# Optimization experiments

Hardware: AMD Instinct MI355X
Metric: run time of the kernel (lower is better)

Reference implementation:

```python
import jax, jax.numpy as jnp
import numpy as np

N = 50000      # nodes
E = 800000     # edges (before self loops)
F_IN = 256     # input features
C = 64         # out_channels per head
H = 4          # heads
NC = 3         # num_class


def setup_inputs() -> dict:
    key = jax.random.key(0)
    ks = jax.random.split(key, 11)
    s = 0.1
    return {
        "x": jax.random.normal(ks[0], (N, F_IN), jnp.float32),
        "edge_index": jax.random.randint(ks[1], (2, E), 0, N, dtype=jnp.int64),
        # conv1: in=F_IN -> H*C, concat
        "W1": jax.random.normal(ks[2], (H * C, F_IN), jnp.float32) * s,
        "as1": jax.random.normal(ks[3], (H, C), jnp.float32) * s,
        "ad1": jax.random.normal(ks[4], (H, C), jnp.float32) * s,
        "b1": jnp.zeros((H * C,), jnp.float32),
        # conv2: in=H*C -> H*C, concat
        "W2": jax.random.normal(ks[5], (H * C, H * C), jnp.float32) * s,
        "as2": jax.random.normal(ks[6], (H, C), jnp.float32) * s,
        "ad2": jax.random.normal(ks[7], (H, C), jnp.float32) * s,
        "b2": jnp.zeros((H * C,), jnp.float32),
        # conv3: in=H*C -> NC, heads averaged (concat=False)
        "W3": jax.random.normal(ks[8], (H * NC, H * C), jnp.float32) * s,
        "as3": jax.random.normal(ks[9], (H, NC), jnp.float32) * s,
        "ad3": jax.random.normal(ks[10], (H, NC), jnp.float32) * s,
        "b3": jnp.zeros((NC,), jnp.float32),
    }


def _gat_conv(x, src, dst, W, a_src, a_dst, b, concat):
    # x: [N,F]; src/dst: [E'] (self loops included); W: [H*C, F]; a_*: [H,C]
    n = x.shape[0]
    h_, c_ = a_src.shape
    h = (x @ W.T).reshape(n, h_, c_)                       # [N,H,C]
    alpha_src = (h * a_src[None]).sum(-1)                  # [N,H]
    alpha_dst = (h * a_dst[None]).sum(-1)                  # [N,H]
    e = jax.nn.leaky_relu(alpha_src[src] + alpha_dst[dst], 0.2)  # [E',H]
    # segment softmax over destination-node neighborhoods
    m = jax.ops.segment_max(e, dst, num_segments=n)        # [N,H]
    ex = jnp.exp(e - m[dst])
    den = jax.ops.segment_sum(ex, dst, num_segments=n)     # [N,H]
    alpha = ex / den[dst]                                  # [E',H]
    out = jax.ops.segment_sum(h[src] * alpha[:, :, None], dst, num_segments=n)  # [N,H,C]
    if concat:
        return out.reshape(n, h_ * c_) + b
    return out.mean(axis=1) + b


def reference(x, edge_index, W1, as1, ad1, b1, W2, as2, ad2, b2, W3, as3, ad3, b3):
    n = x.shape[0]
    loop = jnp.arange(n, dtype=edge_index.dtype)
    src = jnp.concatenate([edge_index[0], loop])  # add_self_loops=True
    dst = jnp.concatenate([edge_index[1], loop])
    x = jax.nn.elu(_gat_conv(x, src, dst, W1, as1, ad1, b1, True))
    x = jax.nn.elu(_gat_conv(x, src, dst, W2, as2, ad2, b2, True))
    x = jax.nn.elu(_gat_conv(x, src, dst, W3, as3, ad3, b3, False))
    return x
```

## Files before the change

kernel.cpp:

```cpp
#include <hip/hip_runtime.h>
#include <hip/hip_fp16.h>
#include <cstdint>
#include <cstddef>

#define NNODES 50000
#define NEDGES 800000
#define E2 (NEDGES + NNODES)
#define HC 256

typedef __attribute__((ext_vector_type(8))) short short8v;
typedef __attribute__((ext_vector_type(4))) float f32x4;


__global__ void zero_int(int* __restrict__ p, int n) {
    int i = blockIdx.x * 256 + threadIdx.x;
    if (i < n) p[i] = 0;
}

__global__ void count_deg(const int* __restrict__ ei, int* __restrict__ deg) {
    int i = blockIdx.x * 256 + threadIdx.x;
    if (i >= E2) return;
    int d = (i < NEDGES) ? ei[NEDGES + i] : (i - NEDGES);
    atomicAdd(&deg[d], 1);
}

__global__ void scan1(const int* __restrict__ deg, int* __restrict__ rp, int* __restrict__ bs) {
    __shared__ int s[256];
    int t = threadIdx.x, i = blockIdx.x * 256 + t;
    int v = (i < NNODES) ? deg[i] : 0;
    s[t] = v;
    __syncthreads();
    for (int o = 1; o < 256; o <<= 1) {
        int add = (t >= o) ? s[t - o] : 0;
        __syncthreads();
        s[t] += add;
        __syncthreads();
    }
    if (i < NNODES) rp[i] = s[t] - v;
    if (t == 255) bs[blockIdx.x] = s[255];
}

__global__ void scan2(int* __restrict__ bs, int nb) {
    __shared__ int s[256];
    int t = threadIdx.x;
    int v = (t < nb) ? bs[t] : 0;
    s[t] = v;
    __syncthreads();
    for (int o = 1; o < 256; o <<= 1) {
        int add = (t >= o) ? s[t - o] : 0;
        __syncthreads();
        s[t] += add;
        __syncthreads();
    }
    bs[t] = s[t] - v;
}

__global__ void scan3(int* __restrict__ rp, const int* __restrict__ bs, int* __restrict__ cnt) {
    int i = blockIdx.x * 256 + threadIdx.x;
    if (i < NNODES) {
        int v = rp[i] + bs[blockIdx.x];
        rp[i] = v;
        cnt[i] = v;
    }
    if (i == 0) rp[NNODES] = E2;
}

__global__ void fill_csr(const int* __restrict__ ei, int* __restrict__ cnt, int* __restrict__ csr) {
    int i = blockIdx.x * 256 + threadIdx.x;
    if (i >= E2) return;
    int s, d;
    if (i < NEDGES) { s = ei[i]; d = ei[NEDGES + i]; }
    else            { s = d = i - NEDGES; }
    int pos = atomicAdd(&cnt[d], 1);
    csr[pos] = s;
}


__device__ __forceinline__ unsigned short f2bf(float f) {
    uint32_t u = __float_as_uint(f);
    uint32_t r = (u + 0x7FFFu + ((u >> 16) & 1u)) >> 16;
    return (unsigned short)r;
}
__device__ __forceinline__ float bf2f(unsigned short h) {
    return __uint_as_float(((uint32_t)h) << 16);
}

__global__ void split_bf16(const float* __restrict__ in, unsigned short* __restrict__ hi,
                           unsigned short* __restrict__ lo, int n4) {
    int i = blockIdx.x * 256 + threadIdx.x;
    if (i >= n4) return;
    float4 v = ((const float4*)in)[i];
    unsigned short h0 = f2bf(v.x), h1 = f2bf(v.y), h2 = f2bf(v.z), h3 = f2bf(v.w);
    unsigned short l0 = f2bf(v.x - bf2f(h0));
    unsigned short l1 = f2bf(v.y - bf2f(h1));
    unsigned short l2 = f2bf(v.z - bf2f(h2));
    unsigned short l3 = f2bf(v.w - bf2f(h3));
    uint2 hp, lp;
    hp.x = (uint32_t)h0 | ((uint32_t)h1 << 16);
    hp.y = (uint32_t)h2 | ((uint32_t)h3 << 16);
    lp.x = (uint32_t)l0 | ((uint32_t)l1 << 16);
    lp.y = (uint32_t)l2 | ((uint32_t)l3 << 16);
    *(uint2*)(hi + 4 * (size_t)i) = hp;
    *(uint2*)(lo + 4 * (size_t)i) = lp;
}


__global__ __launch_bounds__(256, 2) void gemm_mfma(
    const unsigned short* __restrict__ Ah, const unsigned short* __restrict__ Al,
    const unsigned short* __restrict__ Wh, const unsigned short* __restrict__ Wl,
    float* __restrict__ out, _Float16* __restrict__ out16, int M) {
    __shared__ unsigned short sAh[128][32], sAl[128][32], sWh[128][32], sWl[128][32];
    const int t = threadIdx.x;
    const int m0 = blockIdx.x * 128, n0 = blockIdx.y * 128;
    const int lane = t & 63, w = t >> 6;
    const int wr = w >> 1, wc = w & 1;
    const int fr = lane & 15, fg = lane >> 4;

    f32x4 acc[4][4];
#pragma unroll
    for (int mi = 0; mi < 4; mi++)
#pragma unroll
        for (int ni = 0; ni < 4; ni++) acc[mi][ni] = (f32x4){0.f, 0.f, 0.f, 0.f};

    for (int kc = 0; kc < 256; kc += 32) {
#pragma unroll
        for (int i = 0; i < 2; i++) {
            int u = t + 256 * i;
            int row = u >> 2;
            int cb = (u & 3) * 8;
            int gra = m0 + row; gra = gra < M ? gra : M - 1;
            int grw = n0 + row;
            *(short8v*)&sAh[row][cb] = *(const short8v*)(Ah + (size_t)gra * HC + kc + cb);
            *(short8v*)&sAl[row][cb] = *(const short8v*)(Al + (size_t)gra * HC + kc + cb);
            *(short8v*)&sWh[row][cb] = *(const short8v*)(Wh + (size_t)grw * HC + kc + cb);
            *(short8v*)&sWl[row][cb] = *(const short8v*)(Wl + (size_t)grw * HC + kc + cb);
        }
        __syncthreads();

        short8v ah[4], al[4], bh[4], bl[4];
#pragma unroll
        for (int i = 0; i < 4; i++) {
            ah[i] = *(const short8v*)&sAh[wr * 64 + i * 16 + fr][fg * 8];
            al[i] = *(const short8v*)&sAl[wr * 64 + i * 16 + fr][fg * 8];
            bh[i] = *(const short8v*)&sWh[wc * 64 + i * 16 + fr][fg * 8];
            bl[i] = *(const short8v*)&sWl[wc * 64 + i * 16 + fr][fg * 8];
        }
#pragma unroll
        for (int mi = 0; mi < 4; mi++)
#pragma unroll
            for (int ni = 0; ni < 4; ni++) {
                acc[mi][ni] = __builtin_amdgcn_mfma_f32_16x16x32_bf16(ah[mi], bh[ni], acc[mi][ni], 0, 0, 0);
                acc[mi][ni] = __builtin_amdgcn_mfma_f32_16x16x32_bf16(ah[mi], bl[ni], acc[mi][ni], 0, 0, 0);
                acc[mi][ni] = __builtin_amdgcn_mfma_f32_16x16x32_bf16(al[mi], bh[ni], acc[mi][ni], 0, 0, 0);
            }
        __syncthreads();
    }

#pragma unroll
    for (int mi = 0; mi < 4; mi++) {
#pragma unroll
        for (int r = 0; r < 4; r++) {
            int gr = m0 + wr * 64 + mi * 16 + fg * 4 + r;
            if (gr < M) {
#pragma unroll
                for (int ni = 0; ni < 4; ni++) {
                    float v = acc[mi][ni][r];
                    size_t off = (size_t)gr * HC + n0 + wc * 64 + ni * 16 + fr;
                    out[off] = v;
                    out16[off] = (_Float16)v;
                }
            }
        }
    }
}


__global__ void alpha_hc(const float* __restrict__ h, const float* __restrict__ a_s,
                         const float* __restrict__ a_d, float* __restrict__ asrc,
                         float* __restrict__ adst) {
    int n = blockIdx.x;
    int t = threadIdx.x;
    float v = h[(size_t)n * HC + t];
    float ps = v * a_s[t];
    float pd = v * a_d[t];
    for (int o = 32; o > 0; o >>= 1) {
        ps += __shfl_xor(ps, o);
        pd += __shfl_xor(pd, o);
    }
    if ((t & 63) == 0) {
        int w = t >> 6;
        asrc[n * 4 + w] = ps;
        adst[n * 4 + w] = pd;
    }
}


#define CHUNK 512

__global__ void aggregate_hc(const _Float16* __restrict__ h16, const float* __restrict__ asrc,
                             const float* __restrict__ adst, const int* __restrict__ rp,
                             const int* __restrict__ csr, const float* __restrict__ bias,
                             float* __restrict__ y) {
    __shared__ int   sIdx[CHUNK];
    __shared__ float sE[4][CHUNK];
    int n = blockIdx.x;
    int t = threadIdx.x;
    int w = t >> 6, l = t & 63;
    int r0 = rp[n], deg = rp[n + 1] - r0;
    float ad = adst[n * 4 + w];
    int hoff = (w << 6) + l;
    const _Float16* hp = h16 + hoff;

    if (deg <= CHUNK) {
        for (int j = t; j < deg; j += 256) sIdx[j] = csr[r0 + j];
        __syncthreads();

        float m = -1e30f;
        for (int j = l; j < deg; j += 64) {
            int s = sIdx[j];
            float e = asrc[s * 4 + w] + ad;
            e = e > 0.f ? e : 0.2f * e;
            sE[w][j] = e;
            m = fmaxf(m, e);
        }
#pragma unroll
        for (int o = 32; o > 0; o >>= 1) m = fmaxf(m, __shfl_xor(m, o));

        float ssum = 0.f;
        for (int j = l; j < deg; j += 64) {
            float ex = __expf(sE[w][j] - m);
            sE[w][j] = ex;
            ssum += ex;
        }
#pragma unroll
        for (int o = 32; o > 0; o >>= 1) ssum += __shfl_xor(ssum, o);

        float acc = 0.f;
        int j = 0;
        for (; j + 4 <= deg; j += 4) {
            int s0 = sIdx[j], s1 = sIdx[j + 1], s2 = sIdx[j + 2], s3 = sIdx[j + 3];
            float a0 = sE[w][j], a1 = sE[w][j + 1], a2 = sE[w][j + 2], a3 = sE[w][j + 3];
            float h0 = (float)hp[(size_t)s0 * HC];
            float h1 = (float)hp[(size_t)s1 * HC];
            float h2 = (float)hp[(size_t)s2 * HC];
            float h3v = (float)hp[(size_t)s3 * HC];
            acc = fmaf(a0, h0, acc);
            acc = fmaf(a1, h1, acc);
            acc = fmaf(a2, h2, acc);
            acc = fmaf(a3, h3v, acc);
        }
        for (; j < deg; j++) {
            acc = fmaf(sE[w][j], (float)hp[(size_t)sIdx[j] * HC], acc);
        }

        float outv = acc / ssum + bias[hoff];
        outv = outv > 0.f ? outv : expm1f(outv);
        y[(size_t)n * HC + hoff] = outv;
    } else {
        float m = -1e30f;
        for (int j = l; j < deg; j += 64) {
            int s = csr[r0 + j];
            float e = asrc[s * 4 + w] + ad;
            e = e > 0.f ? e : 0.2f * e;
            m = fmaxf(m, e);
        }
#pragma unroll
        for (int o = 32; o > 0; o >>= 1) m = fmaxf(m, __shfl_xor(m, o));

        float acc = 0.f, ssum = 0.f;
        for (int j = 0; j < deg; j++) {
            int s = csr[r0 + j];
            float e = asrc[s * 4 + w] + ad;
            e = e > 0.f ? e : 0.2f * e;
            float a = __expf(e - m);
            ssum += a;
            acc = fmaf(a, (float)hp[(size_t)s * HC], acc);
        }
        float outv = acc / ssum + bias[hoff];
        outv = outv > 0.f ? outv : expm1f(outv);
        y[(size_t)n * HC + hoff] = outv;
    }
}


__global__ void gemm_small(const float* __restrict__ Y, const float* __restrict__ W3,
                           float* __restrict__ h3) {
    int idx = blockIdx.x * 256 + threadIdx.x;
    if (idx >= NNODES * 12) return;
    int n = idx / 12, o = idx - n * 12;
    const float4* xr = (const float4*)(Y + (size_t)n * HC);
    const float4* wr = (const float4*)(W3 + o * HC);
    float acc = 0.f;
#pragma unroll 8
    for (int k = 0; k < 64; k++) {
        float4 a = xr[k], b = wr[k];
        acc += a.x * b.x + a.y * b.y + a.z * b.z + a.w * b.w;
    }
    h3[idx] = acc;
}

__global__ void alpha3(const float* __restrict__ h3, const float* __restrict__ a_s,
                       const float* __restrict__ a_d, float* __restrict__ asrc,
                       float* __restrict__ adst) {
    int n = blockIdx.x * 256 + threadIdx.x;
    if (n >= NNODES) return;
    const float* hr = h3 + (size_t)n * 12;
    float s[4], d[4];
#pragma unroll
    for (int hh = 0; hh < 4; hh++) {
        s[hh] = hr[hh * 3] * a_s[hh * 3] + hr[hh * 3 + 1] * a_s[hh * 3 + 1] + hr[hh * 3 + 2] * a_s[hh * 3 + 2];
        d[hh] = hr[hh * 3] * a_d[hh * 3] + hr[hh * 3 + 1] * a_d[hh * 3 + 1] + hr[hh * 3 + 2] * a_d[hh * 3 + 2];
    }
    *(float4*)(asrc + n * 4) = make_float4(s[0], s[1], s[2], s[3]);
    *(float4*)(adst + n * 4) = make_float4(d[0], d[1], d[2], d[3]);
}

__global__ void aggregate3(const float* __restrict__ h3, const float* __restrict__ asrc,
                           const float* __restrict__ adst, const int* __restrict__ rp,
                           const int* __restrict__ csr, const float* __restrict__ b3,
                           float* __restrict__ out) {
    int n = blockIdx.x * 4 + (threadIdx.x >> 6);
    int l = threadIdx.x & 63;
    if (n >= NNODES) return;
    int r0 = rp[n], deg = rp[n + 1] - r0;
    float4 ad = *(const float4*)(adst + n * 4);

    float m0 = -1e30f, m1 = -1e30f, m2 = -1e30f, m3 = -1e30f;
    for (int j = l; j < deg; j += 64) {
        int s = csr[r0 + j];
        float4 a4 = *(const float4*)(asrc + s * 4);
        float e0 = a4.x + ad.x, e1 = a4.y + ad.y, e2 = a4.z + ad.z, e3 = a4.w + ad.w;
        e0 = e0 > 0.f ? e0 : 0.2f * e0;
        e1 = e1 > 0.f ? e1 : 0.2f * e1;
        e2 = e2 > 0.f ? e2 : 0.2f * e2;
        e3 = e3 > 0.f ? e3 : 0.2f * e3;
        m0 = fmaxf(m0, e0); m1 = fmaxf(m1, e1); m2 = fmaxf(m2, e2); m3 = fmaxf(m3, e3);
    }
    for (int o = 32; o > 0; o >>= 1) {
        m0 = fmaxf(m0, __shfl_xor(m0, o));
        m1 = fmaxf(m1, __shfl_xor(m1, o));
        m2 = fmaxf(m2, __shfl_xor(m2, o));
        m3 = fmaxf(m3, __shfl_xor(m3, o));
    }

    float acc[12];
#pragma unroll
    for (int k = 0; k < 12; k++) acc[k] = 0.f;
    float s0 = 0.f, s1 = 0.f, s2 = 0.f, s3 = 0.f;
    for (int j = l; j < deg; j += 64) {
        int s = csr[r0 + j];
        float4 a4 = *(const float4*)(asrc + s * 4);
        float e0 = a4.x + ad.x, e1 = a4.y + ad.y, e2 = a4.z + ad.z, e3 = a4.w + ad.w;
        e0 = e0 > 0.f ? e0 : 0.2f * e0;
        e1 = e1 > 0.f ? e1 : 0.2f * e1;
        e2 = e2 > 0.f ? e2 : 0.2f * e2;
        e3 = e3 > 0.f ? e3 : 0.2f * e3;
        float w0 = __expf(e0 - m0), w1 = __expf(e1 - m1), w2 = __expf(e2 - m2), w3 = __expf(e3 - m3);
        s0 += w0; s1 += w1; s2 += w2; s3 += w3;
        const float* hr = h3 + (size_t)s * 12;
#pragma unroll
        for (int c = 0; c < 3; c++) {
            acc[c]     += w0 * hr[c];
            acc[3 + c] += w1 * hr[3 + c];
            acc[6 + c] += w2 * hr[6 + c];
            acc[9 + c] += w3 * hr[9 + c];
        }
    }
    for (int o = 32; o > 0; o >>= 1) {
#pragma unroll
        for (int k = 0; k < 12; k++) acc[k] += __shfl_xor(acc[k], o);
        s0 += __shfl_xor(s0, o);
        s1 += __shfl_xor(s1, o);
        s2 += __shfl_xor(s2, o);
        s3 += __shfl_xor(s3, o);
    }
    if (l < 3) {
        float v = 0.25f * (acc[l] / s0 + acc[3 + l] / s1 + acc[6 + l] / s2 + acc[9 + l] / s3) + b3[l];
        v = v > 0.f ? v : expm1f(v);
        out[(size_t)n * 3 + l] = v;
    }
}


extern "C" void kernel_launch(void* const* d_in, const int* in_sizes, int n_in,
                              void* d_out, int out_size, void* d_ws, size_t ws_size,
                              hipStream_t stream) {
    (void)in_sizes; (void)n_in; (void)out_size; (void)ws_size;
    const float* x   = (const float*)d_in[0];
    const int*   ei  = (const int*)d_in[1];
    const float* W1  = (const float*)d_in[2];
    const float* as1 = (const float*)d_in[3];
    const float* ad1 = (const float*)d_in[4];
    const float* b1  = (const float*)d_in[5];
    const float* W2  = (const float*)d_in[6];
    const float* as2 = (const float*)d_in[7];
    const float* ad2 = (const float*)d_in[8];
    const float* b2  = (const float*)d_in[9];
    const float* W3  = (const float*)d_in[10];
    const float* as3 = (const float*)d_in[11];
    const float* ad3 = (const float*)d_in[12];
    const float* b3  = (const float*)d_in[13];
    float* out = (float*)d_out;

    uint8_t* p = (uint8_t*)d_ws;
    auto alloc = [&](size_t bytes) -> void* {
        void* r = (void*)p;
        p += (bytes + 255) & ~(size_t)255;
        return r;
    };
    float* bufH = (float*)alloc((size_t)NNODES * HC * 4);
    float* bufY = (float*)alloc((size_t)NNODES * HC * 4);
    float* h3   = (float*)alloc((size_t)NNODES * 12 * 4);
    float* asrc = (float*)alloc((size_t)NNODES * 4 * 4);
    float* adst = (float*)alloc((size_t)NNODES * 4 * 4);
    int* deg    = (int*)alloc((size_t)NNODES * 4);
    int* rp     = (int*)alloc((size_t)(NNODES + 1) * 4);
    int* cnt    = (int*)alloc((size_t)NNODES * 4);
    int* csr    = (int*)alloc((size_t)E2 * 4);
    int* bsums  = (int*)alloc(256 * 4);
    unsigned short* xh  = (unsigned short*)alloc((size_t)NNODES * HC * 2);
    unsigned short* xl  = (unsigned short*)alloc((size_t)NNODES * HC * 2);
    unsigned short* w1h = (unsigned short*)alloc((size_t)HC * HC * 2);
    unsigned short* w1l = (unsigned short*)alloc((size_t)HC * HC * 2);
    unsigned short* w2h = (unsigned short*)alloc((size_t)HC * HC * 2);
    unsigned short* w2l = (unsigned short*)alloc((size_t)HC * HC * 2);
    _Float16* h16 = (_Float16*)alloc((size_t)NNODES * HC * 2);

    const int NB_N = (NNODES + 255) / 256;
    const int NB_E = (E2 + 255) / 256;
    const int N4_A = NNODES * HC / 4;
    const int N4_W = HC * HC / 4;

    zero_int<<<NB_N, 256, 0, stream>>>(deg, NNODES);
    count_deg<<<NB_E, 256, 0, stream>>>(ei, deg);
    scan1<<<NB_N, 256, 0, stream>>>(deg, rp, bsums);
    scan2<<<1, 256, 0, stream>>>(bsums, NB_N);
    scan3<<<NB_N, 256, 0, stream>>>(rp, bsums, cnt);
    fill_csr<<<NB_E, 256, 0, stream>>>(ei, cnt, csr);

    dim3 ggrid((NNODES + 127) / 128, 2);

    split_bf16<<<(N4_W + 255) / 256, 256, 0, stream>>>(W1, w1h, w1l, N4_W);
    split_bf16<<<(N4_A + 255) / 256, 256, 0, stream>>>(x, xh, xl, N4_A);
    gemm_mfma<<<ggrid, 256, 0, stream>>>(xh, xl, w1h, w1l, bufH, h16, NNODES);
    alpha_hc<<<NNODES, 256, 0, stream>>>(bufH, as1, ad1, asrc, adst);
    aggregate_hc<<<NNODES, 256, 0, stream>>>(h16, asrc, adst, rp, csr, b1, bufY);

    split_bf16<<<(N4_W + 255) / 256, 256, 0, stream>>>(W2, w2h, w2l, N4_W);
    split_bf16<<<(N4_A + 255) / 256, 256, 0, stream>>>(bufY, xh, xl, N4_A);
    gemm_mfma<<<ggrid, 256, 0, stream>>>(xh, xl, w2h, w2l, bufH, h16, NNODES);
    alpha_hc<<<NNODES, 256, 0, stream>>>(bufH, as2, ad2, asrc, adst);
    aggregate_hc<<<NNODES, 256, 0, stream>>>(h16, asrc, adst, rp, csr, b2, bufY);

    gemm_small<<<(NNODES * 12 + 255) / 256, 256, 0, stream>>>(bufY, W3, h3);
    alpha3<<<NB_N, 256, 0, stream>>>(h3, as3, ad3, asrc, adst);
    aggregate3<<<(NNODES + 3) / 4, 256, 0, stream>>>(h3, asrc, adst, rp, csr, b3, out);
}
```

Before: 749.2 us.

## Vectorize aggregation across edges per wave and fuse bf16 split into layer-1 output

The aggregation kernel is restructured so that each wave handles a subset of edges and each lane loads four contiguous fp16 features with one 8-byte read. The four per-wave partials are then reduced through shared memory. The softmax max and sum are computed with all 256 threads spread over heads and edges. Layer 1's aggregation now writes the hi/lo bf16 split directly, which removes the separate split kernel and the fp32 round trip before the layer-2 GEMM. The cost is extra shared memory and block syncs. f2bf/bf2f helpers are assumed to exist in the unseen code.

Measured after the change: 715.4 us. 1.05x faster.

```diff
diff --git a/kernel.cpp b/kernel.cpp
--- a/kernel.cpp
+++ b/kernel.cpp
@@ -200,63 +200,86 @@
 __global__ void aggregate_hc(const _Float16* __restrict__ h16, const float* __restrict__ asrc,
                              const float* __restrict__ adst, const int* __restrict__ rp,
                              const int* __restrict__ csr, const float* __restrict__ bias,
-                             float* __restrict__ y) {
+                             float* __restrict__ y, unsigned short* __restrict__ yh,
+                             unsigned short* __restrict__ yl, int flags) {
     __shared__ int   sIdx[CHUNK];
-    __shared__ float sE[4][CHUNK];
+    __shared__ float sE4[CHUNK][4];
+    __shared__ float sRed[4][64][4];
+    __shared__ float sM[4][4], sS[4][4];
     int n = blockIdx.x;
     int t = threadIdx.x;
-    int w = t >> 6, l = t & 63;
     int r0 = rp[n], deg = rp[n + 1] - r0;
-    float ad = adst[n * 4 + w];
-    int hoff = (w << 6) + l;
-    const _Float16* hp = h16 + hoff;
 
     if (deg <= CHUNK) {
         for (int j = t; j < deg; j += 256) sIdx[j] = csr[r0 + j];
         __syncthreads();
 
-        float m = -1e30f;
-        for (int j = l; j < deg; j += 64) {
+        int hA = t & 3, jj = t >> 2;
+        float adh = adst[n * 4 + hA];
+        float pm = -1e30f;
+        for (int j = jj; j < deg; j += 64) {
             int s = sIdx[j];
-            float e = asrc[s * 4 + w] + ad;
+            float e = asrc[s * 4 + hA] + adh;
             e = e > 0.f ? e : 0.2f * e;
-            sE[w][j] = e;
-            m = fmaxf(m, e);
-        }
-#pragma unroll
-        for (int o = 32; o > 0; o >>= 1) m = fmaxf(m, __shfl_xor(m, o));
-
-        float ssum = 0.f;
-        for (int j = l; j < deg; j += 64) {
-            float ex = __expf(sE[w][j] - m);
-            sE[w][j] = ex;
-            ssum += ex;
-        }
-#pragma unroll
-        for (int o = 32; o > 0; o >>= 1) ssum += __shfl_xor(ssum, o);
-
-        float acc = 0.f;
-        int j = 0;
-        for (; j + 4 <= deg; j += 4) {
-            int s0 = sIdx[j], s1 = sIdx[j + 1], s2 = sIdx[j + 2], s3 = sIdx[j + 3];
-            float a0 = sE[w][j], a1 = sE[w][j + 1], a2 = sE[w][j + 2], a3 = sE[w][j + 3];
-            float h0 = (float)hp[(size_t)s0 * HC];
-            float h1 = (float)hp[(size_t)s1 * HC];
-            float h2 = (float)hp[(size_t)s2 * HC];
-            float h3v = (float)hp[(size_t)s3 * HC];
-            acc = fmaf(a0, h0, acc);
-            acc = fmaf(a1, h1, acc);
-            acc = fmaf(a2, h2, acc);
-            acc = fmaf(a3, h3v, acc);
-        }
-        for (; j < deg; j++) {
-            acc = fmaf(sE[w][j], (float)hp[(size_t)sIdx[j] * HC], acc);
-        }
-
-        float outv = acc / ssum + bias[hoff];
+            sE4[j][hA] = e;
+            pm = fmaxf(pm, e);
+        }
+#pragma unroll
+        for (int o = 4; o <= 32; o <<= 1) pm = fmaxf(pm, __shfl_xor(pm, o));
+        if ((t & 63) < 4) sM[t >> 6][t & 3] = pm;
+        __syncthreads();
+
+        float mh = fmaxf(fmaxf(sM[0][hA], sM[1][hA]), fmaxf(sM[2][hA], sM[3][hA]));
+        float ps = 0.f;
+        for (int j = jj; j < deg; j += 64) {
+            float ex = __expf(sE4[j][hA] - mh);
+            sE4[j][hA] = ex;
+            ps += ex;
+        }
+#pragma unroll
+        for (int o = 4; o <= 32; o <<= 1) ps += __shfl_xor(ps, o);
+        if ((t & 63) < 4) sS[t >> 6][t & 3] = ps;
+        __syncthreads();
+
+        int wv = t >> 6, l = t & 63;
+        int hh = l >> 4;
+        float a0 = 0.f, a1 = 0.f, a2 = 0.f, a3 = 0.f;
+        for (int j = wv; j < deg; j += 4) {
+            int s = sIdx[j];
+            float aw = sE4[j][hh];
+            uint2 raw = *(const uint2*)(h16 + (size_t)s * HC + 4 * l);
+            __half2 p0 = *(__half2*)&raw.x;
+            __half2 p1 = *(__half2*)&raw.y;
+            a0 = fmaf(aw, __low2float(p0), a0);
+            a1 = fmaf(aw, __high2float(p0), a1);
+            a2 = fmaf(aw, __low2float(p1), a2);
+            a3 = fmaf(aw, __high2float(p1), a3);
+        }
+        sRed[wv][l][0] = a0;
+        sRed[wv][l][1] = a1;
+        sRed[wv][l][2] = a2;
+        sRed[wv][l][3] = a3;
+        __syncthreads();
+
+        int c = t;
+        float val = sRed[0][c >> 2][c & 3] + sRed[1][c >> 2][c & 3]
+                  + sRed[2][c >> 2][c & 3] + sRed[3][c >> 2][c & 3];
+        int ch = c >> 6;
+        float ssum = sS[0][ch] + sS[1][ch] + sS[2][ch] + sS[3][ch];
+        float outv = val / ssum + bias[c];
         outv = outv > 0.f ? outv : expm1f(outv);
-        y[(size_t)n * HC + hoff] = outv;
+        size_t off = (size_t)n * HC + c;
+        if (flags & 1) y[off] = outv;
+        if (flags & 2) {
+            unsigned short hi = f2bf(outv);
+            yh[off] = hi;
+            yl[off] = f2bf(outv - bf2f(hi));
+        }
     } else {
+        int w = t >> 6, l = t & 63;
+        float ad = adst[n * 4 + w];
+        int hoff = (w << 6) + l;
+        const _Float16* hp = h16 + hoff;
         float m = -1e30f;
         for (int j = l; j < deg; j += 64) {
             int s = csr[r0 + j];
@@ -266,7 +289,6 @@
         }
 #pragma unroll
         for (int o = 32; o > 0; o >>= 1) m = fmaxf(m, __shfl_xor(m, o));
-
         float acc = 0.f, ssum = 0.f;
         for (int j = 0; j < deg; j++) {
             int s = csr[r0 + j];
@@ -278,7 +300,13 @@
         }
         float outv = acc / ssum + bias[hoff];
         outv = outv > 0.f ? outv : expm1f(outv);
-        y[(size_t)n * HC + hoff] = outv;
+        size_t off = (size_t)n * HC + hoff;
+        if (flags & 1) y[off] = outv;
+        if (flags & 2) {
+            unsigned short hi = f2bf(outv);
+            yh[off] = hi;
+            yl[off] = f2bf(outv - bf2f(hi));
+        }
     }
 }
 
@@ -444,13 +472,12 @@
     split_bf16<<<(N4_A + 255) / 256, 256, 0, stream>>>(x, xh, xl, N4_A);
     gemm_mfma<<<ggrid, 256, 0, stream>>>(xh, xl, w1h, w1l, bufH, h16, NNODES);
     alpha_hc<<<NNODES, 256, 0, stream>>>(bufH, as1, ad1, asrc, adst);
-    aggregate_hc<<<NNODES, 256, 0, stream>>>(h16, asrc, adst, rp, csr, b1, bufY);
+    aggregate_hc<<<NNODES, 256, 0, stream>>>(h16, asrc, adst, rp, csr, b1, bufY, xh, xl, 2);
 
     split_bf16<<<(N4_W + 255) / 256, 256, 0, stream>>>(W2, w2h, w2l, N4_W);
-    split_bf16<<<(N4_A + 255) / 256, 256, 0, stream>>>(bufY, xh, xl, N4_A);
     gemm_mfma<<<ggrid, 256, 0, stream>>>(xh, xl, w2h, w2l, bufH, h16, NNODES);
     alpha_hc<<<NNODES, 256, 0, stream>>>(bufH, as2, ad2, asrc, adst);
-    aggregate_hc<<<NNODES, 256, 0, stream>>>(h16, asrc, adst, rp, csr, b2, bufY);
+    aggregate_hc<<<NNODES, 256, 0, stream>>>(h16, asrc, adst, rp, csr, b2, bufY, xh, xl, 1);
 
     gemm_small<<<(NNODES * 12 + 255) / 256, 256, 0, stream>>>(bufY, W3, h3);
     alpha3<<<NB_N, 256, 0, stream>>>(h3, as3, ad3, asrc, adst);
```
